# Optimization experiments

Measured on AMD Instinct MI355X. Metric: run time of the kernel, lower is better.

Reference implementation:

```python
import jax, jax.numpy as jnp
import numpy as np

N_NODES = 1_000_000
N_EDGES = 32_000_000
DC = 16
HIDDEN = 32
EPS = 1e-8
LN_EPS = 1e-5


def _harmonic_encoding(x, dC):
    # x: [n] curvature in [-1,1]; returns [n, dC] (dC even here)
    norm = jnp.clip((x + 1.0) / (2.0 + EPS), 0.0, 1.0)
    freqs = jnp.arange(1, dC // 2 + 1, dtype=x.dtype) * jnp.pi  # [dC/2]
    ang = norm[:, None] * freqs[None, :]                        # [n, dC/2]
    # interleave sin/cos exactly like torch.stack(...,dim=2).view(n,dC)
    return jnp.stack([jnp.sin(ang), jnp.cos(ang)], axis=2).reshape(x.shape[0], dC)


def setup_inputs() -> dict:
    key = jax.random.key(0)
    k_orc, k_ei, k_w1, k_w2, k_g = jax.random.split(key, 5)
    node_orc = jax.random.uniform(k_orc, (N_NODES,), dtype=jnp.float32) * 2.0 - 1.0
    edge_index = jax.random.randint(k_ei, (2, N_EDGES), 0, N_NODES, dtype=jnp.int64)
    # MLP params (torch Linear convention: W [out, in])
    W1 = jax.random.normal(k_w1, (HIDDEN, DC), dtype=jnp.float32) * (1.0 / np.sqrt(DC))
    b1 = jnp.zeros((HIDDEN,), dtype=jnp.float32)
    W2 = jax.random.normal(k_w2, (DC, HIDDEN), dtype=jnp.float32) * (1.0 / np.sqrt(HIDDEN))
    b2 = jnp.zeros((DC,), dtype=jnp.float32)
    gamma = jnp.ones((DC,), dtype=jnp.float32)
    beta = jnp.zeros((DC,), dtype=jnp.float32)
    return {"node_orc": node_orc, "edge_index": edge_index,
            "W1": W1, "b1": b1, "W2": W2, "b2": b2,
            "gamma": gamma, "beta": beta}


def _neighbor_mean(node_orc, edge_index):
    src, dst = edge_index[0], edge_index[1]
    n = node_orc.shape[0]
    deg = jnp.zeros((n,), node_orc.dtype).at[src].add(1.0).at[dst].add(1.0)
    s = (jnp.zeros((n,), node_orc.dtype)
         .at[src].add(node_orc[dst])
         .at[dst].add(node_orc[src]))
    return jnp.where(deg > 0, s / jnp.where(deg > 0, deg, 1.0), 0.0)


def reference(node_orc, edge_index, W1, b1, W2, b2, gamma, beta):
    # advanced harmonic encoding: node encoding + neighbor-mean encoding
    nb_mean = _neighbor_mean(node_orc, edge_index)
    Phi_base = jnp.concatenate(
        [_harmonic_encoding(node_orc, DC // 2),
         _harmonic_encoding(nb_mean, DC // 2)], axis=1)      # [n, 16]
    # learnable MLP (dropout in eval = identity) + LayerNorm + residual
    h = jax.nn.relu(jnp.einsum('nd,hd->nh', Phi_base, W1) + b1)
    y = jnp.einsum('nh,dh->nd', h, W2) + b2
    mu = jnp.mean(y, axis=-1, keepdims=True)
    var = jnp.var(y, axis=-1, keepdims=True)
    y = (y - mu) / jnp.sqrt(var + LN_EPS) * gamma + beta
    return y + Phi_base
```

## Files before the change

### kernel.cpp

```cpp
#include <hip/hip_runtime.h>

constexpr int kNodes = 1000000;
constexpr int kEdges = 32000000;

constexpr int NB = 256;
constexpr int BSHIFT = 12;
constexpr int BNODES = 4096;
constexpr int NBUSED = (kNodes + BNODES - 1) / BNODES;
constexpr int EPT = 4096;
constexpr int TILES = (kEdges + EPT - 1) / EPT;
constexpr int TSTRIDE = 8960;
constexpr unsigned PADREC = 0x10000000u;
constexpr int SPLIT = 2;

constexpr size_t kRecBytes  = (size_t)TILES * TSTRIDE * 4;
constexpr size_t kTblOff    = kRecBytes;
constexpr size_t kTblBytes  = ((size_t)(NB + 1) * TILES * 2 + 15) & ~(size_t)15;
constexpr size_t kAccOff    = kTblOff + kTblBytes;
constexpr size_t kAccBytes  = (size_t)SPLIT * kNodes * 4;
constexpr size_t kOrcqOff   = kAccOff + kAccBytes;
constexpr size_t kOrcqBytes = (size_t)kNodes * 2;
constexpr size_t kWsNeeded  = kOrcqOff + kOrcqBytes;

__global__ __launch_bounds__(256) void quant_orc(
        const float* __restrict__ orc, unsigned short* __restrict__ orcq) {
    const int i = (blockIdx.x * 256 + threadIdx.x) * 4;
    if (i >= kNodes) return;
    const float4 v = *reinterpret_cast<const float4*>(orc + i);
    unsigned q0 = __float2uint_rn((v.x + 1.0f) * 32768.0f);
    unsigned q1 = __float2uint_rn((v.y + 1.0f) * 32768.0f);
    unsigned q2 = __float2uint_rn((v.z + 1.0f) * 32768.0f);
    unsigned q3 = __float2uint_rn((v.w + 1.0f) * 32768.0f);
    q0 = q0 > 65535u ? 65535u : q0;
    q1 = q1 > 65535u ? 65535u : q1;
    q2 = q2 > 65535u ? 65535u : q2;
    q3 = q3 > 65535u ? 65535u : q3;
    ushort4 q;
    q.x = (unsigned short)q0; q.y = (unsigned short)q1;
    q.z = (unsigned short)q2; q.w = (unsigned short)q3;
    *reinterpret_cast<ushort4*>(orcq + i) = q;
}

__global__ __launch_bounds__(1024) void scatter_sort(
        const int* __restrict__ ei, const unsigned short* __restrict__ orcq,
        unsigned* __restrict__ rec, unsigned short* __restrict__ tbl) {
    __shared__ alignas(16) unsigned reorder[TSTRIDE];
    __shared__ unsigned cnt[NB];
    __shared__ unsigned totsh;
    const int tid = threadIdx.x;
    const int t = blockIdx.x;
    const int e0 = t * EPT;
    const int ne = min(EPT, kEdges - e0);
    const int k4 = tid * 4;

    {
        int4 p4; p4.x = p4.y = p4.z = p4.w = (int)PADREC;
        for (int k = k4; k < TSTRIDE; k += 4096)
            *reinterpret_cast<int4*>(reorder + k) = p4;
    }
    if (tid < NB) cnt[tid] = 0u;
    __syncthreads();

    int4 s4, d4;
    s4.x = s4.y = s4.z = s4.w = 0; d4 = s4;
    unsigned pq0 = 0, pq1 = 0, pq2 = 0, pq3 = 0;
    const bool act = k4 < ne;
    if (act) {
        s4 = *reinterpret_cast<const int4*>(ei + e0 + k4);
        d4 = *reinterpret_cast<const int4*>(ei + kEdges + e0 + k4);
        const unsigned a0 = orcq[d4.x], a1 = orcq[d4.y],
                       a2 = orcq[d4.z], a3 = orcq[d4.w];
        const unsigned b0 = orcq[s4.x], b1 = orcq[s4.y],
                       b2 = orcq[s4.z], b3 = orcq[s4.w];
        atomicAdd(&cnt[(unsigned)s4.x >> BSHIFT], 1u);
        atomicAdd(&cnt[(unsigned)s4.y >> BSHIFT], 1u);
        atomicAdd(&cnt[(unsigned)s4.z >> BSHIFT], 1u);
        atomicAdd(&cnt[(unsigned)s4.w >> BSHIFT], 1u);
        atomicAdd(&cnt[(unsigned)d4.x >> BSHIFT], 1u);
        atomicAdd(&cnt[(unsigned)d4.y >> BSHIFT], 1u);
        atomicAdd(&cnt[(unsigned)d4.z >> BSHIFT], 1u);
        atomicAdd(&cnt[(unsigned)d4.w >> BSHIFT], 1u);
        pq0 = a0 | (b0 << 16);
        pq1 = a1 | (b1 << 16);
        pq2 = a2 | (b2 << 16);
        pq3 = a3 | (b3 << 16);
    }
    __syncthreads();

    if (tid < 64) {
        unsigned c0 = cnt[4 * tid + 0], c1 = cnt[4 * tid + 1];
        unsigned c2 = cnt[4 * tid + 2], c3 = cnt[4 * tid + 3];
        c0 = (c0 + 3u) & ~3u; c1 = (c1 + 3u) & ~3u;
        c2 = (c2 + 3u) & ~3u; c3 = (c3 + 3u) & ~3u;
        const unsigned loc = c0 + c1 + c2 + c3;
        unsigned inc = loc;
        #pragma unroll
        for (int d = 1; d < 64; d <<= 1) {
            const unsigned v = (unsigned)__shfl_up((int)inc, d, 64);
            if (tid >= d) inc += v;
        }
        unsigned base = inc - loc;
        cnt[4 * tid + 0] = base;
        tbl[(size_t)(4 * tid + 0) * TILES + t] = (unsigned short)base;
        base += c0;
        cnt[4 * tid + 1] = base;
        tbl[(size_t)(4 * tid + 1) * TILES + t] = (unsigned short)base;
        base += c1;
        cnt[4 * tid + 2] = base;
        tbl[(size_t)(4 * tid + 2) * TILES + t] = (unsigned short)base;
        base += c2;
        cnt[4 * tid + 3] = base;
        tbl[(size_t)(4 * tid + 3) * TILES + t] = (unsigned short)base;
        if (tid == 63) {
            totsh = inc;
            tbl[(size_t)NB * TILES + t] = (unsigned short)inc;
        }
    }
    __syncthreads();

    if (act) {
        #define RANK1(S, D, PQ) { \
            const unsigned rs_ = atomicAdd(&cnt[(unsigned)(S) >> BSHIFT], 1u); \
            reorder[rs_] = (((unsigned)(S) & (BNODES - 1)) << 16) | ((PQ) & 0xFFFFu); \
            const unsigned rd_ = atomicAdd(&cnt[(unsigned)(D) >> BSHIFT], 1u); \
            reorder[rd_] = (((unsigned)(D) & (BNODES - 1)) << 16) | ((PQ) >> 16); }
        RANK1(s4.x, d4.x, pq0)
        RANK1(s4.y, d4.y, pq1)
        RANK1(s4.z, d4.z, pq2)
        RANK1(s4.w, d4.w, pq3)
        #undef RANK1
    }
    __syncthreads();

    const unsigned total = totsh;
    unsigned* __restrict__ g = rec + (size_t)t * TSTRIDE;
    for (unsigned k = (unsigned)k4; k < total; k += 4096)
        *reinterpret_cast<int4*>(g + k) = *reinterpret_cast<const int4*>(reorder + k);
}

__global__ __launch_bounds__(1024) void bucket_accum(
        const unsigned* __restrict__ rec, const unsigned short* __restrict__ tbl,
        unsigned* __restrict__ acc) {
    __shared__ unsigned lacc[BNODES + 4];
    const int tid = threadIdx.x;
    const int b = blockIdx.x >> 1;
    const int half = blockIdx.x & 1;
    for (int k = tid; k < BNODES + 4; k += 1024) lacc[k] = 0u;
    __syncthreads();
    constexpr int TPS = (TILES + SPLIT - 1) / SPLIT;
    const int t0 = half * TPS;
    const int t1 = min(TILES, t0 + TPS);
    const unsigned short* __restrict__ r0 = tbl + (size_t)b * TILES;
    const unsigned short* __restrict__ r1 = tbl + (size_t)(b + 1) * TILES;
    for (int t = t0 + tid; t < t1; t += 1024) {
        const unsigned st = r0[t];
        const unsigned en = r1[t];
        const uint4* __restrict__ p =
            reinterpret_cast<const uint4*>(rec + (size_t)t * TSTRIDE + st);
        const unsigned n4 = (en - st) >> 2;
        for (unsigned i = 0; i < n4; ++i) {
            const uint4 v = p[i];
            atomicAdd(&lacc[v.x >> 16], (v.x & 0xFFFFu) | 0x1000000u);
            atomicAdd(&lacc[v.y >> 16], (v.y & 0xFFFFu) | 0x1000000u);
            atomicAdd(&lacc[v.z >> 16], (v.z & 0xFFFFu) | 0x1000000u);
            atomicAdd(&lacc[v.w >> 16], (v.w & 0xFFFFu) | 0x1000000u);
        }
    }
    __syncthreads();
    const int base = b << BSHIFT;
    unsigned* __restrict__ dst = acc + (size_t)half * kNodes;
    for (int k = tid; k < BNODES; k += 1024) {
        const int n = base + k;
        if (n < kNodes) dst[n] = lacc[k];
    }
}

constexpr float kScale = 1048576.0f;
constexpr float kInvScale = 1.0f / 1048576.0f;
constexpr long long kBias = 1ll << 36;

__global__ __launch_bounds__(256) void zero_acc(unsigned long long* __restrict__ acc) {
    int i = blockIdx.x * 256 + threadIdx.x;
    if (i < kNodes) acc[i] = 0ull;
}

__global__ __launch_bounds__(256) void edge_kernel(
        const int* __restrict__ ei,
        const float* __restrict__ orc,
        unsigned long long* __restrict__ acc) {
    int t = blockIdx.x * 256 + threadIdx.x;
    int e0 = t * 4;
    if (e0 >= kEdges) return;
    const int4 s4 = *reinterpret_cast<const int4*>(ei + e0);
    const int4 d4 = *reinterpret_cast<const int4*>(ei + kEdges + e0);
    const int ss[4] = {s4.x, s4.y, s4.z, s4.w};
    const int dd[4] = {d4.x, d4.y, d4.z, d4.w};
    #pragma unroll
    for (int k = 0; k < 4; ++k) {
        const float os = orc[ss[k]];
        const float od = orc[dd[k]];
        const unsigned long long ps =
            (1ull << 48) + (unsigned long long)(kBias + (long long)__float2ll_rn(od * kScale));
        const unsigned long long pd =
            (1ull << 48) + (unsigned long long)(kBias + (long long)__float2ll_rn(os * kScale));
        atomicAdd(&acc[ss[k]], ps);
        atomicAdd(&acc[dd[k]], pd);
    }
}

template <int MODE>
__global__ __launch_bounds__(256) void node_kernel(
        const float* __restrict__ orc,
        const unsigned long long* __restrict__ acc64,
        const unsigned* __restrict__ acc32,
        const float* __restrict__ W1, const float* __restrict__ b1,
        const float* __restrict__ W2, const float* __restrict__ b2,
        const float* __restrict__ gamma, const float* __restrict__ beta,
        float* __restrict__ out) {
    const int i = blockIdx.x * 256 + threadIdx.x;
    if (i >= kNodes) return;

    const float x0 = orc[i];
    float nb;
    if (MODE == 0) {
        const unsigned long long p = acc64[i];
        const unsigned deg = (unsigned)(p >> 48);
        const long long sf = (long long)(p & ((1ull << 48) - 1)) - (long long)deg * kBias;
        const float s = (float)sf * kInvScale;
        nb = (deg > 0) ? s / (float)deg : 0.0f;
    } else {
        const unsigned p0 = acc32[i];
        const unsigned p1 = acc32[kNodes + i];
        const unsigned deg = (p0 >> 24) + (p1 >> 24);
        const unsigned sumq = (p0 & 0xFFFFFFu) + (p1 & 0xFFFFFFu);
        nb = (deg > 0)
            ? ((float)sumq * (1.0f / 32768.0f) / (float)deg - 1.0f) : 0.0f;
    }

    constexpr float kPi = 3.14159265358979323846f;
    float Phi[16];
    const float n0 = __saturatef((x0 + 1.0f) * 0.5f);
    const float n1 = __saturatef((nb + 1.0f) * 0.5f);
    #pragma unroll
    for (int k = 0; k < 4; ++k) {
        const float a0 = n0 * (float)(k + 1) * kPi;
        const float a1 = n1 * (float)(k + 1) * kPi;
        Phi[2 * k]     = __sinf(a0);
        Phi[2 * k + 1] = __cosf(a0);
        Phi[8 + 2 * k]     = __sinf(a1);
        Phi[8 + 2 * k + 1] = __cosf(a1);
    }

    float y[16];
    #pragma unroll
    for (int d = 0; d < 16; ++d) y[d] = b2[d];
    #pragma unroll
    for (int j = 0; j < 32; ++j) {
        float a = b1[j];
        #pragma unroll
        for (int d = 0; d < 16; ++d) a = fmaf(Phi[d], W1[j * 16 + d], a);
        a = fmaxf(a, 0.0f);
        #pragma unroll
        for (int d = 0; d < 16; ++d) y[d] = fmaf(a, W2[d * 32 + j], y[d]);
    }

    float mu = 0.0f;
    #pragma unroll
    for (int d = 0; d < 16; ++d) mu += y[d];
    mu *= (1.0f / 16.0f);
    float var = 0.0f;
    #pragma unroll
    for (int d = 0; d < 16; ++d) { const float t = y[d] - mu; var = fmaf(t, t, var); }
    var *= (1.0f / 16.0f);
    const float inv = rsqrtf(var + 1e-5f);

    float4* o4 = reinterpret_cast<float4*>(out + (size_t)i * 16);
    #pragma unroll
    for (int q = 0; q < 4; ++q) {
        float4 o;
        o.x = (y[4 * q + 0] - mu) * inv * gamma[4 * q + 0] + beta[4 * q + 0] + Phi[4 * q + 0];
        o.y = (y[4 * q + 1] - mu) * inv * gamma[4 * q + 1] + beta[4 * q + 1] + Phi[4 * q + 1];
        o.z = (y[4 * q + 2] - mu) * inv * gamma[4 * q + 2] + beta[4 * q + 2] + Phi[4 * q + 2];
        o.w = (y[4 * q + 3] - mu) * inv * gamma[4 * q + 3] + beta[4 * q + 3] + Phi[4 * q + 3];
        o4[q] = o;
    }
}

extern "C" void kernel_launch(void* const* d_in, const int* in_sizes, int n_in,
                              void* d_out, int out_size, void* d_ws, size_t ws_size,
                              hipStream_t stream) {
    const float* orc   = (const float*)d_in[0];
    const int*   ei    = (const int*)d_in[1];
    const float* W1    = (const float*)d_in[2];
    const float* b1    = (const float*)d_in[3];
    const float* W2    = (const float*)d_in[4];
    const float* b2    = (const float*)d_in[5];
    const float* gamma = (const float*)d_in[6];
    const float* beta  = (const float*)d_in[7];
    float* out = (float*)d_out;
    char* ws = (char*)d_ws;

    if (ws_size >= kWsNeeded) {
        unsigned* rec = (unsigned*)ws;
        unsigned short* tbl = (unsigned short*)(ws + kTblOff);
        unsigned* acc = (unsigned*)(ws + kAccOff);
        unsigned short* orcq = (unsigned short*)(ws + kOrcqOff);
        quant_orc<<<(kNodes / 4 + 255) / 256, 256, 0, stream>>>(orc, orcq);
        scatter_sort<<<TILES, 1024, 0, stream>>>(ei, orcq, rec, tbl);
        bucket_accum<<<NBUSED * SPLIT, 1024, 0, stream>>>(rec, tbl, acc);
        node_kernel<3><<<(kNodes + 255) / 256, 256, 0, stream>>>(
            orc, nullptr, acc, W1, b1, W2, b2, gamma, beta, out);
    } else {
        unsigned long long* acc = (unsigned long long*)ws;
        zero_acc<<<(kNodes + 255) / 256, 256, 0, stream>>>(acc);
        edge_kernel<<<(kEdges / 4 + 255) / 256, 256, 0, stream>>>(ei, orc, acc);
        node_kernel<0><<<(kNodes + 255) / 256, 256, 0, stream>>>(
            orc, acc, nullptr, W1, b1, W2, b2, gamma, beta, out);
    }
}
```

Baseline: 724.0 us.

## Replace per-tile padded records with global per-bucket arenas via atomic cursors

Instead of writing each tile's sorted records into a padded per-tile slot with an offset table, each scatter block reserves space in a contiguous per-bucket arena using global atomic cursors and scatters records there. bucket_accum then streams one contiguous arena per bucket, split in halves, with no per-tile table lookups or 4-alignment padding. This removes the tile-table indirection and the padding, and gives contiguous, well-balanced reads in the accumulation stage. In exchange the write-out from scatter_sort becomes a scalar scatter with bucket lookups instead of int4 contiguous stores, and it relies on a fixed per-bucket capacity not overflowing.

```diff
diff --git a/kernel.cpp b/kernel.cpp
--- a/kernel.cpp
+++ b/kernel.cpp
@@ -8,22 +8,24 @@
 constexpr int BNODES = 4096;
 constexpr int NBUSED = (kNodes + BNODES - 1) / BNODES;
 constexpr int EPT = 4096;
+constexpr int RECS = EPT * 2;
 constexpr int TILES = (kEdges + EPT - 1) / EPT;
-constexpr int TSTRIDE = 8960;
-constexpr unsigned PADREC = 0x10000000u;
+constexpr int CAP = 288768;
 constexpr int SPLIT = 2;
 
-constexpr size_t kRecBytes  = (size_t)TILES * TSTRIDE * 4;
-constexpr size_t kTblOff    = kRecBytes;
-constexpr size_t kTblBytes  = ((size_t)(NB + 1) * TILES * 2 + 15) & ~(size_t)15;
-constexpr size_t kAccOff    = kTblOff + kTblBytes;
+constexpr size_t kArenaBytes = (size_t)NBUSED * CAP * 4;
+constexpr size_t kCurOff    = kArenaBytes;
+constexpr size_t kCurBytes  = 1024;
+constexpr size_t kAccOff    = kCurOff + kCurBytes;
 constexpr size_t kAccBytes  = (size_t)SPLIT * kNodes * 4;
 constexpr size_t kOrcqOff   = kAccOff + kAccBytes;
 constexpr size_t kOrcqBytes = (size_t)kNodes * 2;
 constexpr size_t kWsNeeded  = kOrcqOff + kOrcqBytes;
 
 __global__ __launch_bounds__(256) void quant_orc(
-        const float* __restrict__ orc, unsigned short* __restrict__ orcq) {
+        const float* __restrict__ orc, unsigned short* __restrict__ orcq,
+        unsigned* __restrict__ gcur) {
+    if (blockIdx.x == 0 && threadIdx.x < NB) gcur[threadIdx.x] = 0u;
     const int i = (blockIdx.x * 256 + threadIdx.x) * 4;
     if (i >= kNodes) return;
     const float4 v = *reinterpret_cast<const float4*>(orc + i);
@@ -43,9 +45,11 @@
 
 __global__ __launch_bounds__(1024) void scatter_sort(
         const int* __restrict__ ei, const unsigned short* __restrict__ orcq,
-        unsigned* __restrict__ rec, unsigned short* __restrict__ tbl) {
-    __shared__ alignas(16) unsigned reorder[TSTRIDE];
+        unsigned* __restrict__ arena, unsigned* __restrict__ gcur) {
+    __shared__ alignas(16) unsigned reorder[RECS];
+    __shared__ unsigned char bucketOf[RECS];
     __shared__ unsigned cnt[NB];
+    __shared__ unsigned dstadd[NB];
     __shared__ unsigned totsh;
     const int tid = threadIdx.x;
     const int t = blockIdx.x;
@@ -53,11 +57,6 @@
     const int ne = min(EPT, kEdges - e0);
     const int k4 = tid * 4;
 
-    {
-        int4 p4; p4.x = p4.y = p4.z = p4.w = (int)PADREC;
-        for (int k = k4; k < TSTRIDE; k += 4096)
-            *reinterpret_cast<int4*>(reorder + k) = p4;
-    }
     if (tid < NB) cnt[tid] = 0u;
     __syncthreads();
 
@@ -87,11 +86,11 @@
     }
     __syncthreads();
 
+    unsigned st0 = 0, st1 = 0, st2 = 0, st3 = 0;
+    unsigned g0 = 0, g1 = 0, g2 = 0, g3 = 0;
     if (tid < 64) {
-        unsigned c0 = cnt[4 * tid + 0], c1 = cnt[4 * tid + 1];
-        unsigned c2 = cnt[4 * tid + 2], c3 = cnt[4 * tid + 3];
-        c0 = (c0 + 3u) & ~3u; c1 = (c1 + 3u) & ~3u;
-        c2 = (c2 + 3u) & ~3u; c3 = (c3 + 3u) & ~3u;
+        const unsigned c0 = cnt[4 * tid + 0], c1 = cnt[4 * tid + 1];
+        const unsigned c2 = cnt[4 * tid + 2], c3 = cnt[4 * tid + 3];
         const unsigned loc = c0 + c1 + c2 + c3;
         unsigned inc = loc;
         #pragma unroll
@@ -99,31 +98,29 @@
             const unsigned v = (unsigned)__shfl_up((int)inc, d, 64);
             if (tid >= d) inc += v;
         }
-        unsigned base = inc - loc;
-        cnt[4 * tid + 0] = base;
-        tbl[(size_t)(4 * tid + 0) * TILES + t] = (unsigned short)base;
-        base += c0;
-        cnt[4 * tid + 1] = base;
-        tbl[(size_t)(4 * tid + 1) * TILES + t] = (unsigned short)base;
-        base += c1;
-        cnt[4 * tid + 2] = base;
-        tbl[(size_t)(4 * tid + 2) * TILES + t] = (unsigned short)base;
-        base += c2;
-        cnt[4 * tid + 3] = base;
-        tbl[(size_t)(4 * tid + 3) * TILES + t] = (unsigned short)base;
-        if (tid == 63) {
-            totsh = inc;
-            tbl[(size_t)NB * TILES + t] = (unsigned short)inc;
-        }
+        st0 = inc - loc; st1 = st0 + c0; st2 = st1 + c1; st3 = st2 + c2;
+        cnt[4 * tid + 0] = st0;
+        cnt[4 * tid + 1] = st1;
+        cnt[4 * tid + 2] = st2;
+        cnt[4 * tid + 3] = st3;
+        g0 = atomicAdd(&gcur[4 * tid + 0], c0);
+        g1 = atomicAdd(&gcur[4 * tid + 1], c1);
+        g2 = atomicAdd(&gcur[4 * tid + 2], c2);
+        g3 = atomicAdd(&gcur[4 * tid + 3], c3);
+        if (tid == 63) totsh = inc;
     }
     __syncthreads();
 
     if (act) {
         #define RANK1(S, D, PQ) { \
-            const unsigned rs_ = atomicAdd(&cnt[(unsigned)(S) >> BSHIFT], 1u); \
+            const unsigned bs_ = (unsigned)(S) >> BSHIFT; \
+            const unsigned rs_ = atomicAdd(&cnt[bs_], 1u); \
             reorder[rs_] = (((unsigned)(S) & (BNODES - 1)) << 16) | ((PQ) & 0xFFFFu); \
-            const unsigned rd_ = atomicAdd(&cnt[(unsigned)(D) >> BSHIFT], 1u); \
-            reorder[rd_] = (((unsigned)(D) & (BNODES - 1)) << 16) | ((PQ) >> 16); }
+            bucketOf[rs_] = (unsigned char)bs_; \
+            const unsigned bd_ = (unsigned)(D) >> BSHIFT; \
+            const unsigned rd_ = atomicAdd(&cnt[bd_], 1u); \
+            reorder[rd_] = (((unsigned)(D) & (BNODES - 1)) << 16) | ((PQ) >> 16); \
+            bucketOf[rd_] = (unsigned char)bd_; }
         RANK1(s4.x, d4.x, pq0)
         RANK1(s4.y, d4.y, pq1)
         RANK1(s4.z, d4.z, pq2)
@@ -132,46 +129,56 @@
     }
     __syncthreads();
 
+    if (tid < 64) {
+        dstadd[4 * tid + 0] = (unsigned)(4 * tid + 0) * CAP + g0 - st0;
+        dstadd[4 * tid + 1] = (unsigned)(4 * tid + 1) * CAP + g1 - st1;
+        dstadd[4 * tid + 2] = (unsigned)(4 * tid + 2) * CAP + g2 - st2;
+        dstadd[4 * tid + 3] = (unsigned)(4 * tid + 3) * CAP + g3 - st3;
+    }
+    __syncthreads();
+
     const unsigned total = totsh;
-    unsigned* __restrict__ g = rec + (size_t)t * TSTRIDE;
-    for (unsigned k = (unsigned)k4; k < total; k += 4096)
-        *reinterpret_cast<int4*>(g + k) = *reinterpret_cast<const int4*>(reorder + k);
+    for (unsigned k = (unsigned)tid; k < total; k += 1024) {
+        const unsigned r = reorder[k];
+        const unsigned bb = bucketOf[k];
+        arena[dstadd[bb] + k] = r;
+    }
 }
 
 __global__ __launch_bounds__(1024) void bucket_accum(
-        const unsigned* __restrict__ rec, const unsigned short* __restrict__ tbl,
+        const unsigned* __restrict__ arena, const unsigned* __restrict__ gcur,
         unsigned* __restrict__ acc) {
-    __shared__ unsigned lacc[BNODES + 4];
+    __shared__ unsigned lacc[BNODES];
     const int tid = threadIdx.x;
     const int b = blockIdx.x >> 1;
     const int half = blockIdx.x & 1;
-    for (int k = tid; k < BNODES + 4; k += 1024) lacc[k] = 0u;
-    __syncthreads();
-    constexpr int TPS = (TILES + SPLIT - 1) / SPLIT;
-    const int t0 = half * TPS;
-    const int t1 = min(TILES, t0 + TPS);
-    const unsigned short* __restrict__ r0 = tbl + (size_t)b * TILES;
-    const unsigned short* __restrict__ r1 = tbl + (size_t)(b + 1) * TILES;
-    for (int t = t0 + tid; t < t1; t += 1024) {
-        const unsigned st = r0[t];
-        const unsigned en = r1[t];
-        const uint4* __restrict__ p =
-            reinterpret_cast<const uint4*>(rec + (size_t)t * TSTRIDE + st);
-        const unsigned n4 = (en - st) >> 2;
-        for (unsigned i = 0; i < n4; ++i) {
-            const uint4 v = p[i];
-            atomicAdd(&lacc[v.x >> 16], (v.x & 0xFFFFu) | 0x1000000u);
-            atomicAdd(&lacc[v.y >> 16], (v.y & 0xFFFFu) | 0x1000000u);
-            atomicAdd(&lacc[v.z >> 16], (v.z & 0xFFFFu) | 0x1000000u);
-            atomicAdd(&lacc[v.w >> 16], (v.w & 0xFFFFu) | 0x1000000u);
+    for (int k = tid; k < BNODES; k += 1024) lacc[k] = 0u;
+    __syncthreads();
+    const unsigned n = gcur[b];
+    const unsigned n4 = n >> 2;
+    const unsigned h0 = half ? (n4 >> 1) : 0u;
+    const unsigned h1 = half ? n4 : (n4 >> 1);
+    const uint4* __restrict__ p =
+        reinterpret_cast<const uint4*>(arena + (size_t)b * CAP);
+    for (unsigned i = h0 + tid; i < h1; i += 1024) {
+        const uint4 v = p[i];
+        atomicAdd(&lacc[v.x >> 16], (v.x & 0xFFFFu) | 0x1000000u);
+        atomicAdd(&lacc[v.y >> 16], (v.y & 0xFFFFu) | 0x1000000u);
+        atomicAdd(&lacc[v.z >> 16], (v.z & 0xFFFFu) | 0x1000000u);
+        atomicAdd(&lacc[v.w >> 16], (v.w & 0xFFFFu) | 0x1000000u);
+    }
+    if (half) {
+        for (unsigned k = (n4 << 2) + tid; k < n; k += 1024) {
+            const unsigned v = arena[(size_t)b * CAP + k];
+            atomicAdd(&lacc[v >> 16], (v & 0xFFFFu) | 0x1000000u);
         }
     }
     __syncthreads();
     const int base = b << BSHIFT;
     unsigned* __restrict__ dst = acc + (size_t)half * kNodes;
     for (int k = tid; k < BNODES; k += 1024) {
-        const int n = base + k;
-        if (n < kNodes) dst[n] = lacc[k];
+        const int nn = base + k;
+        if (nn < kNodes) dst[nn] = lacc[k];
     }
 }
 
@@ -301,13 +308,13 @@
     char* ws = (char*)d_ws;
 
     if (ws_size >= kWsNeeded) {
-        unsigned* rec = (unsigned*)ws;
-        unsigned short* tbl = (unsigned short*)(ws + kTblOff);
+        unsigned* arena = (unsigned*)ws;
+        unsigned* gcur = (unsigned*)(ws + kCurOff);
         unsigned* acc = (unsigned*)(ws + kAccOff);
         unsigned short* orcq = (unsigned short*)(ws + kOrcqOff);
-        quant_orc<<<(kNodes / 4 + 255) / 256, 256, 0, stream>>>(orc, orcq);
-        scatter_sort<<<TILES, 1024, 0, stream>>>(ei, orcq, rec, tbl);
-        bucket_accum<<<NBUSED * SPLIT, 1024, 0, stream>>>(rec, tbl, acc);
+        quant_orc<<<(kNodes / 4 + 255) / 256, 256, 0, stream>>>(orc, orcq, gcur);
+        scatter_sort<<<TILES, 1024, 0, stream>>>(ei, orcq, arena, gcur);
+        bucket_accum<<<NBUSED * SPLIT, 1024, 0, stream>>>(arena, gcur, acc);
         node_kernel<3><<<(kNodes + 255) / 256, 256, 0, stream>>>(
             orc, nullptr, acc, W1, b1, W2, b2, gamma, beta, out);
     } else {
```

Result: slower. 1.012 ms (+39.8%).

## Pack bucket records densely, transpose offset table, warp-cooperative bucket reads

Applied to the files above, without the earlier changes.

The scatter pass now packs sorted records contiguously per tile without padding each bucket to a multiple of four, and drops the pad-fill of shared memory. The offset table is transposed to tile-major rows, so each tile writes its offsets contiguously. The bucket accumulation switches from one thread per tile reading vectorized runs to one wavefront per tile reading coalesced scalar records. Scatter blocks shrink to 512 threads with 8 edges per thread to raise occupancy, at the cost of narrower loads in the accumulation pass and strided table reads across tiles.

```diff
diff --git a/kernel.cpp b/kernel.cpp
--- a/kernel.cpp
+++ b/kernel.cpp
@@ -8,14 +8,14 @@
 constexpr int BNODES = 4096;
 constexpr int NBUSED = (kNodes + BNODES - 1) / BNODES;
 constexpr int EPT = 4096;
+constexpr int RECS = EPT * 2;
 constexpr int TILES = (kEdges + EPT - 1) / EPT;
-constexpr int TSTRIDE = 8960;
-constexpr unsigned PADREC = 0x10000000u;
+constexpr int TROW = NB + 1;
 constexpr int SPLIT = 2;
 
-constexpr size_t kRecBytes  = (size_t)TILES * TSTRIDE * 4;
+constexpr size_t kRecBytes  = (size_t)TILES * RECS * 4;
 constexpr size_t kTblOff    = kRecBytes;
-constexpr size_t kTblBytes  = ((size_t)(NB + 1) * TILES * 2 + 15) & ~(size_t)15;
+constexpr size_t kTblBytes  = ((size_t)TILES * TROW * 2 + 15) & ~(size_t)15;
 constexpr size_t kAccOff    = kTblOff + kTblBytes;
 constexpr size_t kAccBytes  = (size_t)SPLIT * kNodes * 4;
 constexpr size_t kOrcqOff   = kAccOff + kAccBytes;
@@ -41,137 +41,116 @@
     *reinterpret_cast<ushort4*>(orcq + i) = q;
 }
 
-__global__ __launch_bounds__(1024) void scatter_sort(
+__global__ __launch_bounds__(512, 8) void scatter_sort(
         const int* __restrict__ ei, const unsigned short* __restrict__ orcq,
         unsigned* __restrict__ rec, unsigned short* __restrict__ tbl) {
-    __shared__ alignas(16) unsigned reorder[TSTRIDE];
+    __shared__ alignas(16) unsigned reorder[RECS];
     __shared__ unsigned cnt[NB];
-    __shared__ unsigned totsh;
     const int tid = threadIdx.x;
     const int t = blockIdx.x;
     const int e0 = t * EPT;
     const int ne = min(EPT, kEdges - e0);
-    const int k4 = tid * 4;
-
-    {
-        int4 p4; p4.x = p4.y = p4.z = p4.w = (int)PADREC;
-        for (int k = k4; k < TSTRIDE; k += 4096)
-            *reinterpret_cast<int4*>(reorder + k) = p4;
-    }
+    const int k8 = tid * 8;
+
     if (tid < NB) cnt[tid] = 0u;
     __syncthreads();
 
-    int4 s4, d4;
-    s4.x = s4.y = s4.z = s4.w = 0; d4 = s4;
-    unsigned pq0 = 0, pq1 = 0, pq2 = 0, pq3 = 0;
-    const bool act = k4 < ne;
+    int s[8], d[8];
+    unsigned pq[8];
+    const bool act = k8 < ne;
     if (act) {
-        s4 = *reinterpret_cast<const int4*>(ei + e0 + k4);
-        d4 = *reinterpret_cast<const int4*>(ei + kEdges + e0 + k4);
-        const unsigned a0 = orcq[d4.x], a1 = orcq[d4.y],
-                       a2 = orcq[d4.z], a3 = orcq[d4.w];
-        const unsigned b0 = orcq[s4.x], b1 = orcq[s4.y],
-                       b2 = orcq[s4.z], b3 = orcq[s4.w];
-        atomicAdd(&cnt[(unsigned)s4.x >> BSHIFT], 1u);
-        atomicAdd(&cnt[(unsigned)s4.y >> BSHIFT], 1u);
-        atomicAdd(&cnt[(unsigned)s4.z >> BSHIFT], 1u);
-        atomicAdd(&cnt[(unsigned)s4.w >> BSHIFT], 1u);
-        atomicAdd(&cnt[(unsigned)d4.x >> BSHIFT], 1u);
-        atomicAdd(&cnt[(unsigned)d4.y >> BSHIFT], 1u);
-        atomicAdd(&cnt[(unsigned)d4.z >> BSHIFT], 1u);
-        atomicAdd(&cnt[(unsigned)d4.w >> BSHIFT], 1u);
-        pq0 = a0 | (b0 << 16);
-        pq1 = a1 | (b1 << 16);
-        pq2 = a2 | (b2 << 16);
-        pq3 = a3 | (b3 << 16);
+        const int4 sa = *reinterpret_cast<const int4*>(ei + e0 + k8);
+        const int4 sb = *reinterpret_cast<const int4*>(ei + e0 + k8 + 4);
+        const int4 da = *reinterpret_cast<const int4*>(ei + kEdges + e0 + k8);
+        const int4 db = *reinterpret_cast<const int4*>(ei + kEdges + e0 + k8 + 4);
+        s[0] = sa.x; s[1] = sa.y; s[2] = sa.z; s[3] = sa.w;
+        s[4] = sb.x; s[5] = sb.y; s[6] = sb.z; s[7] = sb.w;
+        d[0] = da.x; d[1] = da.y; d[2] = da.z; d[3] = da.w;
+        d[4] = db.x; d[5] = db.y; d[6] = db.z; d[7] = db.w;
+        #pragma unroll
+        for (int j = 0; j < 8; ++j) {
+            const unsigned a = orcq[d[j]];
+            const unsigned b = orcq[s[j]];
+            pq[j] = a | (b << 16);
+        }
+        #pragma unroll
+        for (int j = 0; j < 8; ++j) {
+            atomicAdd(&cnt[(unsigned)s[j] >> BSHIFT], 1u);
+            atomicAdd(&cnt[(unsigned)d[j] >> BSHIFT], 1u);
+        }
     }
     __syncthreads();
 
     if (tid < 64) {
-        unsigned c0 = cnt[4 * tid + 0], c1 = cnt[4 * tid + 1];
-        unsigned c2 = cnt[4 * tid + 2], c3 = cnt[4 * tid + 3];
-        c0 = (c0 + 3u) & ~3u; c1 = (c1 + 3u) & ~3u;
-        c2 = (c2 + 3u) & ~3u; c3 = (c3 + 3u) & ~3u;
+        const unsigned c0 = cnt[4 * tid + 0], c1 = cnt[4 * tid + 1];
+        const unsigned c2 = cnt[4 * tid + 2], c3 = cnt[4 * tid + 3];
         const unsigned loc = c0 + c1 + c2 + c3;
         unsigned inc = loc;
         #pragma unroll
-        for (int d = 1; d < 64; d <<= 1) {
-            const unsigned v = (unsigned)__shfl_up((int)inc, d, 64);
-            if (tid >= d) inc += v;
-        }
+        for (int o = 1; o < 64; o <<= 1) {
+            const unsigned v = (unsigned)__shfl_up((int)inc, o, 64);
+            if (tid >= o) inc += v;
+        }
+        unsigned short* __restrict__ row = tbl + (size_t)t * TROW;
         unsigned base = inc - loc;
-        cnt[4 * tid + 0] = base;
-        tbl[(size_t)(4 * tid + 0) * TILES + t] = (unsigned short)base;
+        cnt[4 * tid + 0] = base; row[4 * tid + 0] = (unsigned short)base;
         base += c0;
-        cnt[4 * tid + 1] = base;
-        tbl[(size_t)(4 * tid + 1) * TILES + t] = (unsigned short)base;
+        cnt[4 * tid + 1] = base; row[4 * tid + 1] = (unsigned short)base;
         base += c1;
-        cnt[4 * tid + 2] = base;
-        tbl[(size_t)(4 * tid + 2) * TILES + t] = (unsigned short)base;
+        cnt[4 * tid + 2] = base; row[4 * tid + 2] = (unsigned short)base;
         base += c2;
-        cnt[4 * tid + 3] = base;
-        tbl[(size_t)(4 * tid + 3) * TILES + t] = (unsigned short)base;
-        if (tid == 63) {
-            totsh = inc;
-            tbl[(size_t)NB * TILES + t] = (unsigned short)inc;
-        }
+        cnt[4 * tid + 3] = base; row[4 * tid + 3] = (unsigned short)base;
+        if (tid == 63) row[NB] = (unsigned short)(2 * ne);
     }
     __syncthreads();
 
     if (act) {
-        #define RANK1(S, D, PQ) { \
-            const unsigned rs_ = atomicAdd(&cnt[(unsigned)(S) >> BSHIFT], 1u); \
-            reorder[rs_] = (((unsigned)(S) & (BNODES - 1)) << 16) | ((PQ) & 0xFFFFu); \
-            const unsigned rd_ = atomicAdd(&cnt[(unsigned)(D) >> BSHIFT], 1u); \
-            reorder[rd_] = (((unsigned)(D) & (BNODES - 1)) << 16) | ((PQ) >> 16); }
-        RANK1(s4.x, d4.x, pq0)
-        RANK1(s4.y, d4.y, pq1)
-        RANK1(s4.z, d4.z, pq2)
-        RANK1(s4.w, d4.w, pq3)
-        #undef RANK1
-    }
-    __syncthreads();
-
-    const unsigned total = totsh;
-    unsigned* __restrict__ g = rec + (size_t)t * TSTRIDE;
-    for (unsigned k = (unsigned)k4; k < total; k += 4096)
+        #pragma unroll
+        for (int j = 0; j < 8; ++j) {
+            const unsigned rs = atomicAdd(&cnt[(unsigned)s[j] >> BSHIFT], 1u);
+            reorder[rs] = (((unsigned)s[j] & (BNODES - 1)) << 16) | (pq[j] & 0xFFFFu);
+            const unsigned rd = atomicAdd(&cnt[(unsigned)d[j] >> BSHIFT], 1u);
+            reorder[rd] = (((unsigned)d[j] & (BNODES - 1)) << 16) | (pq[j] >> 16);
+        }
+    }
+    __syncthreads();
+
+    const int tot = 2 * ne;
+    unsigned* __restrict__ g = rec + (size_t)t * RECS;
+    for (int k = tid * 4; k < tot; k += 2048)
         *reinterpret_cast<int4*>(g + k) = *reinterpret_cast<const int4*>(reorder + k);
 }
 
 __global__ __launch_bounds__(1024) void bucket_accum(
         const unsigned* __restrict__ rec, const unsigned short* __restrict__ tbl,
         unsigned* __restrict__ acc) {
-    __shared__ unsigned lacc[BNODES + 4];
+    __shared__ unsigned lacc[BNODES];
     const int tid = threadIdx.x;
     const int b = blockIdx.x >> 1;
     const int half = blockIdx.x & 1;
-    for (int k = tid; k < BNODES + 4; k += 1024) lacc[k] = 0u;
+    for (int k = tid; k < BNODES; k += 1024) lacc[k] = 0u;
     __syncthreads();
     constexpr int TPS = (TILES + SPLIT - 1) / SPLIT;
     const int t0 = half * TPS;
     const int t1 = min(TILES, t0 + TPS);
-    const unsigned short* __restrict__ r0 = tbl + (size_t)b * TILES;
-    const unsigned short* __restrict__ r1 = tbl + (size_t)(b + 1) * TILES;
-    for (int t = t0 + tid; t < t1; t += 1024) {
-        const unsigned st = r0[t];
-        const unsigned en = r1[t];
-        const uint4* __restrict__ p =
-            reinterpret_cast<const uint4*>(rec + (size_t)t * TSTRIDE + st);
-        const unsigned n4 = (en - st) >> 2;
-        for (unsigned i = 0; i < n4; ++i) {
-            const uint4 v = p[i];
-            atomicAdd(&lacc[v.x >> 16], (v.x & 0xFFFFu) | 0x1000000u);
-            atomicAdd(&lacc[v.y >> 16], (v.y & 0xFFFFu) | 0x1000000u);
-            atomicAdd(&lacc[v.z >> 16], (v.z & 0xFFFFu) | 0x1000000u);
-            atomicAdd(&lacc[v.w >> 16], (v.w & 0xFFFFu) | 0x1000000u);
+    const int wid = tid >> 6;
+    const int lane = tid & 63;
+    for (int t = t0 + wid; t < t1; t += 16) {
+        const unsigned short* __restrict__ row = tbl + (size_t)t * TROW + b;
+        const unsigned st = row[0];
+        const unsigned en = row[1];
+        const unsigned* __restrict__ p = rec + (size_t)t * RECS;
+        for (unsigned k = st + lane; k < en; k += 64) {
+            const unsigned v = p[k];
+            atomicAdd(&lacc[v >> 16], (v & 0xFFFFu) | 0x1000000u);
         }
     }
     __syncthreads();
     const int base = b << BSHIFT;
     unsigned* __restrict__ dst = acc + (size_t)half * kNodes;
     for (int k = tid; k < BNODES; k += 1024) {
-        const int n = base + k;
-        if (n < kNodes) dst[n] = lacc[k];
+        const int nn = base + k;
+        if (nn < kNodes) dst[nn] = lacc[k];
     }
 }
 
@@ -306,7 +285,7 @@
         unsigned* acc = (unsigned*)(ws + kAccOff);
         unsigned short* orcq = (unsigned short*)(ws + kOrcqOff);
         quant_orc<<<(kNodes / 4 + 255) / 256, 256, 0, stream>>>(orc, orcq);
-        scatter_sort<<<TILES, 1024, 0, stream>>>(ei, orcq, rec, tbl);
+        scatter_sort<<<TILES, 512, 0, stream>>>(ei, orcq, rec, tbl);
         bucket_accum<<<NBUSED * SPLIT, 1024, 0, stream>>>(rec, tbl, acc);
         node_kernel<3><<<(kNodes + 255) / 256, 256, 0, stream>>>(
             orc, nullptr, acc, W1, b1, W2, b2, gamma, beta, out);
```

Result: slower. 902.9 us (+24.7%).
